# Optimization experiments

Hardware: AMD Instinct MI355X
Metric: run time of the kernel (lower is better)

The kernel has to match this reference:

```python
import jax, jax.numpy as jnp
import numpy as np

WINDOW = (2, 7, 7)
SHIFT = (1, 3, 3)
HEADS = 4


def _rel_pos_index(ws):
    coords = np.stack(np.meshgrid(*[np.arange(w) for w in ws], indexing='ij'))  # (3, wd, wh, ww)
    cf = coords.reshape(3, -1)
    rel = cf[:, :, None] - cf[:, None, :]  # (3, N, N)
    rel = rel.transpose(1, 2, 0).astype(np.int64)
    rel[:, :, 0] += ws[0] - 1
    rel[:, :, 1] += ws[1] - 1
    rel[:, :, 2] += ws[2] - 1
    rel[:, :, 0] *= (2 * ws[1] - 1) * (2 * ws[2] - 1)
    rel[:, :, 1] *= 2 * ws[2] - 1
    return rel.sum(-1)  # (N, N)


def _attn_mask(D, H, W, ws, ss):
    img = np.zeros((1, D, H, W, 1), np.float32)
    cnt = 0
    for d in (slice(None, -ws[0]), slice(-ws[0], -ss[0]), slice(-ss[0], None)):
        for h in (slice(None, -ws[1]), slice(-ws[1], -ss[1]), slice(-ss[1], None)):
            for w in (slice(None, -ws[2]), slice(-ws[2], -ss[2]), slice(-ss[2], None)):
                img[:, d, h, w, :] = cnt
                cnt += 1
    N = ws[0] * ws[1] * ws[2]
    mw = img.reshape(1, D // ws[0], ws[0], H // ws[1], ws[1], W // ws[2], ws[2], 1)
    mw = mw.transpose(0, 1, 3, 5, 2, 4, 6, 7).reshape(-1, N)  # (nW, N)
    diff = mw[:, None, :] - mw[:, :, None]
    return np.where(diff != 0, -100.0, 0.0).astype(np.float32)  # (nW, N, N)


def _win_partition(x, ws):
    B, D, H, W, C = x.shape
    x = x.reshape(B, D // ws[0], ws[0], H // ws[1], ws[1], W // ws[2], ws[2], C)
    return x.transpose(0, 1, 3, 5, 2, 4, 6, 7).reshape(-1, ws[0] * ws[1] * ws[2], C)


def _win_reverse(win, ws, B, D, H, W):
    C = win.shape[-1]
    x = win.reshape(B, D // ws[0], H // ws[1], W // ws[2], ws[0], ws[1], ws[2], C)
    return x.transpose(0, 1, 4, 2, 5, 3, 6, 7).reshape(B, D, H, W, C)


def _ln(x, w, b):
    mu = x.mean(-1, keepdims=True)
    var = x.var(-1, keepdims=True)
    return (x - mu) / jnp.sqrt(var + 1e-5) * w + b


def setup_inputs() -> dict:
    key = jax.random.key(0)
    ks = jax.random.split(key, 8)
    B, D, H, W, C = 4, 8, 56, 56, 128
    hidden = 4 * C
    table = (2 * WINDOW[0] - 1) * (2 * WINDOW[1] - 1) * (2 * WINDOW[2] - 1)
    return {
        'x': jax.random.normal(ks[0], (B, D, H, W, C), jnp.float32),
        'norm1_w': jnp.ones((C,), jnp.float32),
        'norm1_b': jnp.zeros((C,), jnp.float32),
        'qkv_w': 0.02 * jax.random.normal(ks[1], (3 * C, C), jnp.float32),
        'qkv_b': jnp.zeros((3 * C,), jnp.float32),
        'rpb': 0.02 * jax.random.normal(ks[2], (table, HEADS), jnp.float32),
        'proj_w': 0.02 * jax.random.normal(ks[3], (C, C), jnp.float32),
        'proj_b': jnp.zeros((C,), jnp.float32),
        'norm2_w': jnp.ones((C,), jnp.float32),
        'norm2_b': jnp.zeros((C,), jnp.float32),
        'fc1_w': 0.02 * jax.random.normal(ks[4], (hidden, C), jnp.float32),
        'fc1_b': jnp.zeros((hidden,), jnp.float32),
        'fc2_w': 0.02 * jax.random.normal(ks[5], (C, hidden), jnp.float32),
        'fc2_b': jnp.zeros((C,), jnp.float32),
    }


def reference(x, norm1_w, norm1_b, qkv_w, qkv_b, rpb, proj_w, proj_b,
              norm2_w, norm2_b, fc1_w, fc1_b, fc2_w, fc2_b):
    B, D, H, W, C = x.shape
    hd = C // HEADS
    scale = hd ** -0.5
    N = WINDOW[0] * WINDOW[1] * WINDOW[2]

    shortcut = x
    y = _ln(x, norm1_w, norm1_b)
    # cyclic shift (SW-MSA)
    y = jnp.roll(y, (-SHIFT[0], -SHIFT[1], -SHIFT[2]), axis=(1, 2, 3))
    win = _win_partition(y, WINDOW)  # (B_, N, C)
    B_ = win.shape[0]

    qkv = win @ qkv_w.T + qkv_b  # (B_, N, 3C)
    qkv = qkv.reshape(B_, N, 3, HEADS, hd).transpose(2, 0, 3, 1, 4)
    q, k, v = qkv[0] * scale, qkv[1], qkv[2]  # (B_, h, N, hd)

    attn = jnp.einsum('bhnd,bhmd->bhnm', q, k)  # (B_, h, N, N)
    rpi = _rel_pos_index(WINDOW)
    bias = rpb[rpi.reshape(-1)].reshape(N, N, HEADS).transpose(2, 0, 1)  # (h, N, N)
    attn = attn + bias[None]

    mask = jnp.asarray(_attn_mask(D, H, W, WINDOW, SHIFT))  # (nW, N, N)
    nW = mask.shape[0]
    attn = attn.reshape(B_ // nW, nW, HEADS, N, N) + mask[None, :, None]
    attn = jax.nn.softmax(attn.reshape(B_, HEADS, N, N), axis=-1)

    out = jnp.einsum('bhnm,bhmd->bhnd', attn, v)
    out = out.transpose(0, 2, 1, 3).reshape(B_, N, C)
    out = out @ proj_w.T + proj_b

    y = _win_reverse(out, WINDOW, B, D, H, W)
    y = jnp.roll(y, SHIFT, axis=(1, 2, 3))  # reverse cyclic shift
    x = shortcut + y

    h = _ln(x, norm2_w, norm2_b)
    h = jax.nn.gelu(h @ fc1_w.T + fc1_b, approximate=False)
    h = h @ fc2_w.T + fc2_b
    return x + h
```

## Files before the change

### kernel.cpp

```cpp
#include <hip/hip_runtime.h>
#include <math.h>

typedef short bf16x8 __attribute__((ext_vector_type(8)));
typedef float f32x4 __attribute__((ext_vector_type(4)));
typedef unsigned short u16;

#define DEVFN static __device__ __forceinline__

DEVFN u16 f2bf(float f) {
  union { float f; unsigned u; } v; v.f = f;
  return (u16)((v.u + 0x7FFFu + ((v.u >> 16) & 1u)) >> 16);
}

DEVFN void gload16(const void* g, void* l) {
  __builtin_amdgcn_global_load_lds(
      (const __attribute__((address_space(1))) void*)g,
      (__attribute__((address_space(3))) void*)l, 16, 0, 0);
}

DEVFN float gelu_fast(float x) {
  float e = __expf(-1.702f * x);
  return x * __builtin_amdgcn_rcpf(1.0f + e);
}

#define TT 100352
#define BWIN 1024

__global__ void convert4_kernel(const float* __restrict__ a, const float* __restrict__ b,
                                const float* __restrict__ c, const float* __restrict__ d,
                                u16* __restrict__ oa, u16* __restrict__ ob,
                                u16* __restrict__ oc, u16* __restrict__ od) {
  int i = blockIdx.x * 256 + threadIdx.x;
  const float* s; u16* o; int off;
  if (i < 49152)       { s = a; o = oa; off = i; }
  else if (i < 65536)  { s = b; o = ob; off = i - 49152; }
  else if (i < 131072) { s = c; o = oc; off = i - 65536; }
  else                 { s = d; o = od; off = i - 131072; }
  o[off] = f2bf(s[off]);
}

__global__ void biasmask_kernel(const float* __restrict__ rpb, float* __restrict__ bm) {
  int idx = blockIdx.x * 256 + threadIdx.x;
  int lane = idx & 63;
  int rem = idx >> 6;
  int nt = rem % 7;  rem /= 7;
  int mt = rem % 7;  rem /= 7;
  int h = rem & 3;
  int pat = rem >> 2;
  int dB = (pat >> 2) & 1, hB = (pat >> 1) & 1, wB = pat & 1;
  int jc = nt * 16 + (lane & 15);
  f32x4 out;
  #pragma unroll
  for (int r = 0; r < 4; ++r) {
    int ic = mt * 16 + (lane >> 4) * 4 + r;
    float v;
    if (jc > 97) v = -30000.f;
    else if (ic > 97) v = 0.f;
    else {
      int di = ic / 49, ri = ic % 49, hi = ri / 7, wi = ri % 7;
      int dj = jc / 49, rj = jc % 49, hj = rj / 7, wj = rj % 7;
      int tidx = (di - dj + 1) * 169 + (hi - hj + 6) * 13 + (wi - wj + 6);
      v = rpb[tidx * 4 + h];
      int ridi = (dB ? (di == 0 ? 1 : 2) * 9 : 0) + (hB ? (hi < 4 ? 1 : 2) * 3 : 0)
               + (wB ? (wi < 4 ? 1 : 2) : 0);
      int ridj = (dB ? (dj == 0 ? 1 : 2) * 9 : 0) + (hB ? (hj < 4 ? 1 : 2) * 3 : 0)
               + (wB ? (wj < 4 ? 1 : 2) : 0);
      if (ridi != ridj) v -= 100.f;
    }
    out[r] = v;
  }
  *(f32x4*)(bm + (size_t)idx * 4) = out;
}

__global__ __launch_bounds__(256) void ln_kernel(const float* __restrict__ x,
    const float* __restrict__ w, const float* __restrict__ bterm, u16* __restrict__ out)
{
  int gw = blockIdx.x * 4 + (threadIdx.x >> 6);
  int lane = threadIdx.x & 63;
  int b_ = gw / 98, n = gw % 98;
  int bb = b_ >> 8, widx = b_ & 255;
  int dw = widx >> 6, hw = (widx >> 3) & 7, ww = widx & 7;
  int dd = n / 49, rr = n % 49, hh = rr / 7, wn = rr % 7;
  int d = (dw * 2 + dd + 1) & 7;
  int h = hw * 7 + hh + 3; if (h >= 56) h -= 56;
  int wq = ww * 7 + wn + 3; if (wq >= 56) wq -= 56;
  size_t src = ((size_t)(((bb * 8 + d) * 56 + h) * 56 + wq)) * 128;
  float2 v = *(const float2*)(x + src + lane * 2);
  float s = v.x + v.y, q = v.x * v.x + v.y * v.y;
  #pragma unroll
  for (int m = 1; m < 64; m <<= 1) { s += __shfl_xor(s, m, 64); q += __shfl_xor(q, m, 64); }
  float mu = s * (1.0f / 128.0f);
  float var = q * (1.0f / 128.0f) - mu * mu;
  float rstd = rsqrtf(var + 1e-5f);
  int c = lane * 2;
  float y0 = (v.x - mu) * rstd * w[c] + bterm[c];
  float y1 = (v.y - mu) * rstd * w[c + 1] + bterm[c + 1];
  ushort2 o; o.x = f2bf(y0); o.y = f2bf(y1);
  *(ushort2*)(out + (size_t)gw * 128 + c) = o;
}

template<int EPI>
__global__ __launch_bounds__(256) void gemm_kernel(
    const u16* __restrict__ A, const u16* __restrict__ Bw,
    const float* __restrict__ bias, const float* __restrict__ res,
    void* __restrict__ outp, const float* __restrict__ n2w,
    const float* __restrict__ n2b, u16* __restrict__ h1out,
    int M, int N, int K)
{
  __shared__ u16 smem[EPI == 1 ? 17664 : 16384];
  u16* As = smem;
  u16* Bs = smem + 8192;
  const int m0 = blockIdx.x * 128, n0 = blockIdx.y * 128;
  const int t = threadIdx.x;
  const int wid = t >> 6, lane = t & 63;
  const int wr = wid >> 1, wc = wid & 1;
  const int l15 = lane & 15, lhi = lane >> 4;
  const int srow = lane >> 3;
  const int sslot = lane & 7;
  const int gcol = ((sslot ^ srow) << 3);
  f32x4 acc[4][4] = {};
  for (int k0 = 0; k0 < K; k0 += 64) {
    #pragma unroll
    for (int it = 0; it < 4; ++it) {
      const int rbase = it * 32 + wid * 8;
      const int row = rbase + srow;
      gload16(A + (size_t)(m0 + row) * K + k0 + gcol, As + rbase * 64);
      gload16(Bw + (size_t)(n0 + row) * K + k0 + gcol, Bs + rbase * 64);
    }
    __syncthreads();
    #pragma unroll
    for (int kk = 0; kk < 64; kk += 32) {
      bf16x8 af[4], bfr[4];
      const int csw = (kk + lhi * 8) ^ ((l15 & 7) << 3);
      #pragma unroll
      for (int mi = 0; mi < 4; ++mi) af[mi] = *(const bf16x8*)(As + (wr * 64 + mi * 16 + l15) * 64 + csw);
      #pragma unroll
      for (int ni = 0; ni < 4; ++ni) bfr[ni] = *(const bf16x8*)(Bs + (wc * 64 + ni * 16 + l15) * 64 + csw);
      #pragma unroll
      for (int mi = 0; mi < 4; ++mi)
        #pragma unroll
        for (int ni = 0; ni < 4; ++ni)
          acc[mi][ni] = __builtin_amdgcn_mfma_f32_16x16x32_bf16(af[mi], bfr[ni], acc[mi][ni], 0, 0, 0);
    }
    __syncthreads();
  }
  if (EPI == 0) {
    const float smul = (n0 == 0) ? 0.17677669529663689f : 1.0f;
    #pragma unroll
    for (int mi = 0; mi < 4; ++mi)
      #pragma unroll
      for (int ni = 0; ni < 4; ++ni) {
        int col = wc * 64 + ni * 16 + l15;
        float bcol = bias[n0 + col];
        #pragma unroll
        for (int r = 0; r < 4; ++r) {
          int row = wr * 64 + mi * 16 + lhi * 4 + r;
          float v = (acc[mi][ni][r] + bcol) * smul;
          smem[row * 128 + (((col >> 3) ^ (row & 7)) << 3) + (col & 7)] = f2bf(v);
        }
      }
    __syncthreads();
    const int rsub = t >> 4, sl = t & 15;
    #pragma unroll
    for (int j = 0; j < 8; ++j) {
      int row = j * 16 + rsub;
      int4 val = *(const int4*)(smem + row * 128 + ((sl ^ (row & 7)) << 3));
      *(int4*)((u16*)outp + (size_t)(m0 + row) * N + n0 + sl * 8) = val;
    }
  } else {
    float* Pk = (float*)smem;
    #pragma unroll
    for (int half = 0; half < 2; ++half) {
      if (wr == half) {
        #pragma unroll
        for (int ni = 0; ni < 4; ++ni) {
          int col = wc * 64 + ni * 16 + l15;
          float bcol = bias[col];
          #pragma unroll
          for (int mi = 0; mi < 4; ++mi)
            #pragma unroll
            for (int r = 0; r < 4; ++r)
              Pk[(mi * 16 + lhi * 4 + r) * 138 + col] = acc[mi][ni][r] + bcol;
        }
      }
      __syncthreads();
      {
        int rowl = t >> 2, q = t & 3;
        int grow = m0 + half * 64 + rowl;
        int b_ = grow / 98, n = grow % 98;
        int bb = b_ >> 8, widx = b_ & 255;
        int dw = widx >> 6, hw = (widx >> 3) & 7, ww = widx & 7;
        int dd = n / 49, rr = n % 49, hh = rr / 7, wn = rr % 7;
        int d = (dw * 2 + dd + 1) & 7;
        int hq = hw * 7 + hh + 3; if (hq >= 56) hq -= 56;
        int wq = ww * 7 + wn + 3; if (wq >= 56) wq -= 56;
        size_t dbase = ((size_t)(((bb * 8 + d) * 56 + hq) * 56 + wq)) * 128;
        f32x4 vals[8];
        float s = 0.f, sq = 0.f;
        #pragma unroll
        for (int j = 0; j < 8; ++j) {
          int col = j * 16 + q * 4;
          f32x4 pv = *(const f32x4*)(Pk + rowl * 138 + col);
          f32x4 rv = *(const f32x4*)(res + dbase + col);
          f32x4 v = pv + rv;
          vals[j] = v;
          *(f32x4*)((float*)outp + dbase + col) = v;
          s += v[0] + v[1] + v[2] + v[3];
          sq += v[0]*v[0] + v[1]*v[1] + v[2]*v[2] + v[3]*v[3];
        }
        s += __shfl_xor(s, 1, 64);  sq += __shfl_xor(sq, 1, 64);
        s += __shfl_xor(s, 2, 64);  sq += __shfl_xor(sq, 2, 64);
        float mu = s * (1.0f / 128.0f);
        float var = sq * (1.0f / 128.0f) - mu * mu;
        float rstd = rsqrtf(var + 1e-5f);
        #pragma unroll
        for (int j = 0; j < 8; ++j) {
          int col = j * 16 + q * 4;
          f32x4 wv = *(const f32x4*)(n2w + col);
          f32x4 bv = *(const f32x4*)(n2b + col);
          u16 hb[4];
          #pragma unroll
          for (int e = 0; e < 4; ++e)
            hb[e] = f2bf((vals[j][e] - mu) * rstd * wv[e] + bv[e]);
          *(int2*)(h1out + dbase + col) = *(const int2*)hb;
        }
      }
      __syncthreads();
    }
  }
}

__global__ __launch_bounds__(256, 2) void mlp_kernel(
    const u16* __restrict__ A, const u16* __restrict__ W1, const float* __restrict__ b1,
    const u16* __restrict__ W2, const float* __restrict__ b2,
    const float* __restrict__ res, float* __restrict__ outp)
{
  __shared__ u16 smem[34816];
  u16* W1c = smem;
  u16* W2c = smem + 8192;
  u16* HsA = smem + 24576;
  float* b1s = (float*)(smem + 33792);
  float* Pk = (float*)smem;
  const int m0 = blockIdx.x * 128;
  const int t = threadIdx.x, wid = t >> 6, lane = t & 63;
  const int l15 = lane & 15, lhi = lane >> 4;
  const int srow4 = lane >> 4, sslot16 = lane & 15;
  const int srow8 = lane >> 3, sslot8 = lane & 7;
  u16* hs = HsA + wid * 2304;

  #pragma unroll
  for (int it = 0; it < 4; ++it) {
    int rb1 = it * 16 + wid * 4, r1 = rb1 + srow4;
    gload16(W1 + (size_t)r1 * 128 + ((sslot16 ^ (r1 & 7)) << 3), W1c + rb1 * 128);
    int rb2 = it * 32 + wid * 8, r2 = rb2 + srow8;
    gload16(W2 + (size_t)r2 * 512 + ((sslot8 ^ (r2 & 7)) << 3), W2c + rb2 * 64);
  }
  if (t < 128) *(f32x4*)(b1s + t * 4) = *(const f32x4*)(b1 + t * 4);
  bf16x8 areg[2][4];
  #pragma unroll
  for (int mi = 0; mi < 2; ++mi)
    #pragma unroll
    for (int kg = 0; kg < 4; ++kg)
      areg[mi][kg] = *(const bf16x8*)(A + (size_t)(m0 + wid * 32 + mi * 16 + l15) * 128 + kg * 32 + lhi * 8);

  f32x4 accO[2][8] = {};
  __syncthreads();
  for (int hc = 0; hc < 8; ++hc) {
    const int cur = (hc & 1) * 8192;
    if (hc < 7) {
      const int nxt = ((hc + 1) & 1) * 8192;
      #pragma unroll
      for (int it = 0; it < 4; ++it) {
        int rb2 = it * 32 + wid * 8, r2 = rb2 + srow8;
        gload16(W2 + (size_t)r2 * 512 + (hc + 1) * 64 + ((sslot8 ^ (r2 & 7)) << 3),
                W2c + nxt + rb2 * 64);
      }
    }
    f32x4 accH[2][4] = {};
    #pragma unroll
    for (int kk = 0; kk < 4; ++kk) {
      bf16x8 bw[4];
      #pragma unroll
      for (int ni = 0; ni < 4; ++ni) {
        int row = ni * 16 + l15;
        bw[ni] = *(const bf16x8*)(W1c + row * 128 + (((kk * 4 + lhi) ^ (row & 7)) << 3));
      }
      #pragma unroll
      for (int mi = 0; mi < 2; ++mi)
        #pragma unroll
        for (int ni = 0; ni < 4; ++ni)
          accH[mi][ni] = __builtin_amdgcn_mfma_f32_16x16x32_bf16(areg[mi][kk], bw[ni], accH[mi][ni], 0, 0, 0);
    }
    #pragma unroll
    for (int mi = 0; mi < 2; ++mi)
      #pragma unroll
      for (int ni = 0; ni < 4; ++ni) {
        float bb = b1s[hc * 64 + ni * 16 + l15];
        #pragma unroll
        for (int r = 0; r < 4; ++r) {
          int tokl = mi * 16 + lhi * 4 + r;
          hs[tokl * 72 + ni * 16 + l15] = f2bf(gelu_fast(accH[mi][ni][r] + bb));
        }
      }
    __syncthreads();
    if (hc < 7) {
      #pragma unroll
      for (int it = 0; it < 4; ++it) {
        int rb1 = it * 16 + wid * 4, r1 = rb1 + srow4;
        gload16(W1 + (size_t)((hc + 1) * 64 + r1) * 128 + ((sslot16 ^ (r1 & 7)) << 3),
                W1c + rb1 * 128);
      }
    }
    #pragma unroll
    for (int kk = 0; kk < 2; ++kk) {
      bf16x8 ah[2], bw2[8];
      #pragma unroll
      for (int mi = 0; mi < 2; ++mi)
        ah[mi] = *(const bf16x8*)(hs + (mi * 16 + l15) * 72 + kk * 32 + lhi * 8);
      #pragma unroll
      for (int ni = 0; ni < 8; ++ni) {
        int row = ni * 16 + l15;
        bw2[ni] = *(const bf16x8*)(W2c + cur + row * 64 + (((kk * 4 + lhi) ^ (row & 7)) << 3));
      }
      #pragma unroll
      for (int mi = 0; mi < 2; ++mi)
        #pragma unroll
        for (int ni = 0; ni < 8; ++ni)
          accO[mi][ni] = __builtin_amdgcn_mfma_f32_16x16x32_bf16(ah[mi], bw2[ni], accO[mi][ni], 0, 0, 0);
    }
    __syncthreads();
  }
  #pragma unroll
  for (int half = 0; half < 2; ++half) {
    if ((wid >> 1) == half) {
      #pragma unroll
      for (int ni = 0; ni < 8; ++ni) {
        int col = ni * 16 + l15;
        float bv = b2[col];
        #pragma unroll
        for (int mi = 0; mi < 2; ++mi)
          #pragma unroll
          for (int r = 0; r < 4; ++r) {
            int tokl = (wid & 1) * 32 + mi * 16 + lhi * 4 + r;
            Pk[tokl * 132 + col] = accO[mi][ni][r] + bv;
          }
      }
    }
    __syncthreads();
    #pragma unroll
    for (int p = 0; p < 8; ++p) {
      int idx = p * 256 + t;
      int row = idx >> 5, c = (idx & 31) * 4;
      size_t gtok = (size_t)(m0 + half * 64 + row);
      f32x4 v = *(const f32x4*)(Pk + row * 132 + c);
      f32x4 rv = *(const f32x4*)(res + gtok * 128 + c);
      *(f32x4*)(outp + gtok * 128 + c) = v + rv;
    }
    __syncthreads();
  }
}

__global__ __launch_bounds__(64) void attn_kernel(
    const u16* __restrict__ qkv, const float* __restrict__ biasmask,
    u16* __restrict__ out_win)
{
  __shared__ u16 vT[32][136];
  __shared__ u16 P[16][136];
  const int bid = blockIdx.x;
  const int w = bid >> 2, h = bid & 3;
  const int lane = threadIdx.x;
  const int l15 = lane & 15, lhi = lane >> 4;
  const int widx = w & 255;
  const int dw = widx >> 6, hw = (widx >> 3) & 7, ww = widx & 7;
  const int pat = ((dw == 3) ? 4 : 0) | ((hw == 7) ? 2 : 0) | ((ww == 7) ? 1 : 0);
  const float* bmh = biasmask + (size_t)(pat * 4 + h) * (49 * 256);

  for (int f = lane; f < 160; f += 64) {
    int d = f / 5, c = 96 + (f % 5) * 8;
    *(int4*)&vT[d][c] = (int4){0, 0, 0, 0};
  }
  if (lane < 48) {
    int r = lane / 3, c = 112 + (lane % 3) * 8;
    *(int4*)&P[r][c] = (int4){0, 0, 0, 0};
  }
  const size_t base = (size_t)w * 98 * 384;
  for (int f = lane; f < 392; f += 64) {
    int n = f >> 2, c = (f & 3) * 8;
    int4 v = *(const int4*)(qkv + base + (size_t)n * 384 + 256 + h * 32 + c);
    const u16* pv = (const u16*)&v;
    #pragma unroll
    for (int j = 0; j < 8; ++j) vT[c + j][n] = pv[j];
  }
  const size_t obase = (size_t)w * 98 * 128;
  for (int mt = 0; mt < 7; ++mt) {
    int qn = mt * 16 + l15; if (qn > 97) qn = 97;
    bf16x8 aq = *(const bf16x8*)(qkv + base + (size_t)qn * 384 + h * 32 + lhi * 8);
    f32x4 sf[7];
    #pragma unroll
    for (int nt = 0; nt < 7; ++nt) {
      int kn = nt * 16 + l15; if (kn > 97) kn = 97;
      bf16x8 bk = *(const bf16x8*)(qkv + base + (size_t)kn * 384 + 128 + h * 32 + lhi * 8);
      f32x4 z = {0.f, 0.f, 0.f, 0.f};
      sf[nt] = __builtin_amdgcn_mfma_f32_16x16x32_bf16(aq, bk, z, 0, 0, 0);
    }
    float mx[4] = {-1e30f, -1e30f, -1e30f, -1e30f};
    #pragma unroll
    for (int nt = 0; nt < 7; ++nt) {
      f32x4 bm = *(const f32x4*)(bmh + (mt * 7 + nt) * 256 + lane * 4);
      #pragma unroll
      for (int r = 0; r < 4; ++r) {
        float s = sf[nt][r] + bm[r];
        sf[nt][r] = s;
        mx[r] = fmaxf(mx[r], s);
      }
    }
    #pragma unroll
    for (int m = 1; m < 16; m <<= 1)
      #pragma unroll
      for (int r = 0; r < 4; ++r) mx[r] = fmaxf(mx[r], __shfl_xor(mx[r], m, 64));
    float sm[4] = {0.f, 0.f, 0.f, 0.f};
    #pragma unroll
    for (int nt = 0; nt < 7; ++nt)
      #pragma unroll
      for (int r = 0; r < 4; ++r) {
        float p = __expf(sf[nt][r] - mx[r]);
        sf[nt][r] = p;
        sm[r] += p;
      }
    #pragma unroll
    for (int m = 1; m < 16; m <<= 1)
      #pragma unroll
      for (int r = 0; r < 4; ++r) sm[r] += __shfl_xor(sm[r], m, 64);
    float inv[4];
    #pragma unroll
    for (int r = 0; r < 4; ++r) inv[r] = 1.0f / sm[r];
    #pragma unroll
    for (int nt = 0; nt < 7; ++nt)
      #pragma unroll
      for (int r = 0; r < 4; ++r)
        P[lhi * 4 + r][nt * 16 + l15] = f2bf(sf[nt][r] * inv[r]);
    f32x4 o0 = {}, o1 = {};
    #pragma unroll
    for (int ks = 0; ks < 4; ++ks) {
      bf16x8 ap  = *(const bf16x8*)(&P[l15][ks * 32 + lhi * 8]);
      bf16x8 bv0 = *(const bf16x8*)(&vT[l15][ks * 32 + lhi * 8]);
      bf16x8 bv1 = *(const bf16x8*)(&vT[16 + l15][ks * 32 + lhi * 8]);
      o0 = __builtin_amdgcn_mfma_f32_16x16x32_bf16(ap, bv0, o0, 0, 0, 0);
      o1 = __builtin_amdgcn_mfma_f32_16x16x32_bf16(ap, bv1, o1, 0, 0, 0);
    }
    int irow0 = mt * 16 + lhi * 4;
    #pragma unroll
    for (int r = 0; r < 4; ++r) {
      if (irow0 + r < 98) {
        size_t orow = obase + (size_t)(irow0 + r) * 128 + h * 32;
        out_win[orow + l15] = f2bf(o0[r]);
        out_win[orow + 16 + l15] = f2bf(o1[r]);
      }
    }
  }
}

extern "C" void kernel_launch(void* const* d_in, const int* in_sizes, int n_in,
                              void* d_out, int out_size, void* d_ws, size_t ws_size,
                              hipStream_t stream)
{
  const float* x      = (const float*)d_in[0];
  const float* n1w    = (const float*)d_in[1];
  const float* n1b    = (const float*)d_in[2];
  const float* qkv_w  = (const float*)d_in[3];
  const float* qkv_b  = (const float*)d_in[4];
  const float* rpb    = (const float*)d_in[5];
  const float* proj_w = (const float*)d_in[6];
  const float* proj_b = (const float*)d_in[7];
  const float* n2w    = (const float*)d_in[8];
  const float* n2b    = (const float*)d_in[9];
  const float* fc1_w  = (const float*)d_in[10];
  const float* fc1_b  = (const float*)d_in[11];
  const float* fc2_w  = (const float*)d_in[12];
  const float* fc2_b  = (const float*)d_in[13];

  char* p = (char*)d_ws;
  size_t off = 0;
  auto alloc = [&](size_t bytes) { void* r = p + off; off = (off + bytes + 255) & ~(size_t)255; return r; };
  u16*   qkvw_b    = (u16*)alloc(49152 * 2);
  u16*   projw_b   = (u16*)alloc(16384 * 2);
  u16*   fc1w_b    = (u16*)alloc(65536 * 2);
  u16*   fc2w_b    = (u16*)alloc(65536 * 2);
  float* biasmask  = (float*)alloc(8 * 4 * 49 * 256 * 4);
  u16*   y_win     = (u16*)alloc((size_t)TT * 128 * 2);
  float* x2        = (float*)alloc((size_t)TT * 128 * 4);
  u16*   h1        = (u16*)alloc((size_t)TT * 128 * 2);
  u16*   big       = (u16*)alloc((size_t)TT * 384 * 2);
  if (off > ws_size) return;

  convert4_kernel<<<768, 256, 0, stream>>>(qkv_w, proj_w, fc1_w, fc2_w,
                                           qkvw_b, projw_b, fc1w_b, fc2w_b);
  biasmask_kernel<<<392, 256, 0, stream>>>(rpb, biasmask);
  ln_kernel<<<TT / 4, 256, 0, stream>>>(x, n1w, n1b, y_win);
  gemm_kernel<0><<<dim3(TT / 128, 3), 256, 0, stream>>>(y_win, qkvw_b, qkv_b, nullptr, big,
                                                        nullptr, nullptr, nullptr, TT, 384, 128);
  attn_kernel<<<BWIN * 4, 64, 0, stream>>>(big, biasmask, y_win);
  gemm_kernel<1><<<dim3(TT / 128, 1), 256, 0, stream>>>(y_win, projw_b, proj_b, x, x2,
                                                        n2w, n2b, h1, TT, 128, 128);
  mlp_kernel<<<TT / 128, 256, 0, stream>>>(h1, fc1w_b, fc1_b, fc2w_b, fc2_b, x2, (float*)d_out);
}
```

Before: 199.7 us.

## Fuse LayerNorm1 into QKV GEMM and store residual x2 in bf16

Removes the standalone LayerNorm kernel: the QKV GEMM now gathers the shifted-window rows of x, normalizes them in registers and writes the bf16 A tile directly into shared memory. Each of the three column blocks recomputes the same LayerNorm, trading extra fp32 reads of x for skipping a separate pass and the y_win round trip. Separately, the intermediate residual x2 is stored as bf16 instead of fp32, halving its write and read traffic at a precision cost in the final residual add.

```diff
diff --git a/kernel.cpp b/kernel.cpp
--- a/kernel.cpp
+++ b/kernel.cpp
@@ -10,6 +10,11 @@
 DEVFN u16 f2bf(float f) {
   union { float f; unsigned u; } v; v.f = f;
   return (u16)((v.u + 0x7FFFu + ((v.u >> 16) & 1u)) >> 16);
+}
+
+DEVFN float bf2f(u16 u) {
+  union { unsigned u; float f; } v; v.u = ((unsigned)u) << 16;
+  return v.f;
 }
 
 DEVFN void gload16(const void* g, void* l) {
@@ -72,44 +77,13 @@
   *(f32x4*)(bm + (size_t)idx * 4) = out;
 }
 
-__global__ __launch_bounds__(256) void ln_kernel(const float* __restrict__ x,
-    const float* __restrict__ w, const float* __restrict__ bterm, u16* __restrict__ out)
+__global__ __launch_bounds__(256) void qkv_kernel(
+    const float* __restrict__ x, const float* __restrict__ n1w, const float* __restrict__ n1b,
+    const u16* __restrict__ Bw, const float* __restrict__ bias, u16* __restrict__ outp)
 {
-  int gw = blockIdx.x * 4 + (threadIdx.x >> 6);
-  int lane = threadIdx.x & 63;
-  int b_ = gw / 98, n = gw % 98;
-  int bb = b_ >> 8, widx = b_ & 255;
-  int dw = widx >> 6, hw = (widx >> 3) & 7, ww = widx & 7;
-  int dd = n / 49, rr = n % 49, hh = rr / 7, wn = rr % 7;
-  int d = (dw * 2 + dd + 1) & 7;
-  int h = hw * 7 + hh + 3; if (h >= 56) h -= 56;
-  int wq = ww * 7 + wn + 3; if (wq >= 56) wq -= 56;
-  size_t src = ((size_t)(((bb * 8 + d) * 56 + h) * 56 + wq)) * 128;
-  float2 v = *(const float2*)(x + src + lane * 2);
-  float s = v.x + v.y, q = v.x * v.x + v.y * v.y;
-  #pragma unroll
-  for (int m = 1; m < 64; m <<= 1) { s += __shfl_xor(s, m, 64); q += __shfl_xor(q, m, 64); }
-  float mu = s * (1.0f / 128.0f);
-  float var = q * (1.0f / 128.0f) - mu * mu;
-  float rstd = rsqrtf(var + 1e-5f);
-  int c = lane * 2;
-  float y0 = (v.x - mu) * rstd * w[c] + bterm[c];
-  float y1 = (v.y - mu) * rstd * w[c + 1] + bterm[c + 1];
-  ushort2 o; o.x = f2bf(y0); o.y = f2bf(y1);
-  *(ushort2*)(out + (size_t)gw * 128 + c) = o;
-}
-
-template<int EPI>
-__global__ __launch_bounds__(256) void gemm_kernel(
-    const u16* __restrict__ A, const u16* __restrict__ Bw,
-    const float* __restrict__ bias, const float* __restrict__ res,
-    void* __restrict__ outp, const float* __restrict__ n2w,
-    const float* __restrict__ n2b, u16* __restrict__ h1out,
-    int M, int N, int K)
-{
-  __shared__ u16 smem[EPI == 1 ? 17664 : 16384];
+  __shared__ u16 smem[24576];
   u16* As = smem;
-  u16* Bs = smem + 8192;
+  u16* Bs = smem + 16384;
   const int m0 = blockIdx.x * 128, n0 = blockIdx.y * 128;
   const int t = threadIdx.x;
   const int wid = t >> 6, lane = t & 63;
@@ -118,14 +92,127 @@
   const int srow = lane >> 3;
   const int sslot = lane & 7;
   const int gcol = ((sslot ^ srow) << 3);
+
+  {
+    const int rowl = t >> 1, half = t & 1;
+    const int grow = m0 + rowl;
+    int b_ = grow / 98, n = grow % 98;
+    int bb = b_ >> 8, widx = b_ & 255;
+    int dwv = widx >> 6, hwv = (widx >> 3) & 7, wwv = widx & 7;
+    int dd = n / 49, rr = n % 49, hh = rr / 7, wn = rr % 7;
+    int d = (dwv * 2 + dd + 1) & 7;
+    int hq = hwv * 7 + hh + 3; if (hq >= 56) hq -= 56;
+    int wq = wwv * 7 + wn + 3; if (wq >= 56) wq -= 56;
+    size_t src = ((size_t)(((bb * 8 + d) * 56 + hq) * 56 + wq)) * 128 + half * 64;
+    f32x4 vals[16];
+    float s = 0.f, sq = 0.f;
+    #pragma unroll
+    for (int j = 0; j < 16; ++j) {
+      f32x4 v = *(const f32x4*)(x + src + j * 4);
+      vals[j] = v;
+      s += v[0] + v[1] + v[2] + v[3];
+      sq += v[0]*v[0] + v[1]*v[1] + v[2]*v[2] + v[3]*v[3];
+    }
+    s += __shfl_xor(s, 1, 64);  sq += __shfl_xor(sq, 1, 64);
+    float mu = s * (1.0f / 128.0f);
+    float var = sq * (1.0f / 128.0f) - mu * mu;
+    float rstd = rsqrtf(var + 1e-5f);
+    #pragma unroll
+    for (int j = 0; j < 8; ++j) {
+      int col = half * 64 + j * 8;
+      f32x4 wv0 = *(const f32x4*)(n1w + col);
+      f32x4 wv1 = *(const f32x4*)(n1w + col + 4);
+      f32x4 bv0 = *(const f32x4*)(n1b + col);
+      f32x4 bv1 = *(const f32x4*)(n1b + col + 4);
+      u16 hb[8];
+      #pragma unroll
+      for (int e = 0; e < 4; ++e) {
+        hb[e]     = f2bf((vals[2*j][e]   - mu) * rstd * wv0[e] + bv0[e]);
+        hb[e + 4] = f2bf((vals[2*j+1][e] - mu) * rstd * wv1[e] + bv1[e]);
+      }
+      *(bf16x8*)(As + rowl * 128 + ((((col >> 3) ^ (rowl & 7))) << 3)) = *(const bf16x8*)hb;
+    }
+  }
+
   f32x4 acc[4][4] = {};
-  for (int k0 = 0; k0 < K; k0 += 64) {
+  for (int k0 = 0; k0 < 128; k0 += 64) {
     #pragma unroll
     for (int it = 0; it < 4; ++it) {
       const int rbase = it * 32 + wid * 8;
       const int row = rbase + srow;
-      gload16(A + (size_t)(m0 + row) * K + k0 + gcol, As + rbase * 64);
-      gload16(Bw + (size_t)(n0 + row) * K + k0 + gcol, Bs + rbase * 64);
+      gload16(Bw + (size_t)(n0 + row) * 128 + k0 + gcol, Bs + rbase * 64);
+    }
+    __syncthreads();
+    #pragma unroll
+    for (int kk = 0; kk < 64; kk += 32) {
+      bf16x8 af[4], bfr[4];
+      const int cg = ((k0 + kk) >> 3) + lhi;
+      const int csw = (kk + lhi * 8) ^ ((l15 & 7) << 3);
+      #pragma unroll
+      for (int mi = 0; mi < 4; ++mi) {
+        int row = wr * 64 + mi * 16 + l15;
+        af[mi] = *(const bf16x8*)(As + row * 128 + ((cg ^ (row & 7)) << 3));
+      }
+      #pragma unroll
+      for (int ni = 0; ni < 4; ++ni)
+        bfr[ni] = *(const bf16x8*)(Bs + (wc * 64 + ni * 16 + l15) * 64 + csw);
+      #pragma unroll
+      for (int mi = 0; mi < 4; ++mi)
+        #pragma unroll
+        for (int ni = 0; ni < 4; ++ni)
+          acc[mi][ni] = __builtin_amdgcn_mfma_f32_16x16x32_bf16(af[mi], bfr[ni], acc[mi][ni], 0, 0, 0);
+    }
+    __syncthreads();
+  }
+  const float smul = (n0 == 0) ? 0.17677669529663689f : 1.0f;
+  #pragma unroll
+  for (int mi = 0; mi < 4; ++mi)
+    #pragma unroll
+    for (int ni = 0; ni < 4; ++ni) {
+      int col = wc * 64 + ni * 16 + l15;
+      float bcol = bias[n0 + col];
+      #pragma unroll
+      for (int r = 0; r < 4; ++r) {
+        int row = wr * 64 + mi * 16 + lhi * 4 + r;
+        float v = (acc[mi][ni][r] + bcol) * smul;
+        smem[row * 128 + (((col >> 3) ^ (row & 7)) << 3) + (col & 7)] = f2bf(v);
+      }
+    }
+  __syncthreads();
+  const int rsub = t >> 4, sl = t & 15;
+  #pragma unroll
+  for (int j = 0; j < 8; ++j) {
+    int row = j * 16 + rsub;
+    int4 val = *(const int4*)(smem + row * 128 + ((sl ^ (row & 7)) << 3));
+    *(int4*)(outp + (size_t)(m0 + row) * 384 + n0 + sl * 8) = val;
+  }
+}
+
+__global__ __launch_bounds__(256) void proj_kernel(
+    const u16* __restrict__ A, const u16* __restrict__ Bw,
+    const float* __restrict__ bias, const float* __restrict__ res,
+    u16* __restrict__ x2out, const float* __restrict__ n2w,
+    const float* __restrict__ n2b, u16* __restrict__ h1out)
+{
+  __shared__ u16 smem[17664];
+  u16* As = smem;
+  u16* Bs = smem + 8192;
+  const int m0 = blockIdx.x * 128;
+  const int t = threadIdx.x;
+  const int wid = t >> 6, lane = t & 63;
+  const int wr = wid >> 1, wc = wid & 1;
+  const int l15 = lane & 15, lhi = lane >> 4;
+  const int srow = lane >> 3;
+  const int sslot = lane & 7;
+  const int gcol = ((sslot ^ srow) << 3);
+  f32x4 acc[4][4] = {};
+  for (int k0 = 0; k0 < 128; k0 += 64) {
+    #pragma unroll
+    for (int it = 0; it < 4; ++it) {
+      const int rbase = it * 32 + wid * 8;
+      const int row = rbase + srow;
+      gload16(A + (size_t)(m0 + row) * 128 + k0 + gcol, As + rbase * 64);
+      gload16(Bw + (size_t)row * 128 + k0 + gcol, Bs + rbase * 64);
     }
     __syncthreads();
     #pragma unroll
@@ -144,96 +231,73 @@
     }
     __syncthreads();
   }
-  if (EPI == 0) {
-    const float smul = (n0 == 0) ? 0.17677669529663689f : 1.0f;
-    #pragma unroll
-    for (int mi = 0; mi < 4; ++mi)
+  float* Pk = (float*)smem;
+  #pragma unroll
+  for (int half = 0; half < 2; ++half) {
+    if (wr == half) {
       #pragma unroll
       for (int ni = 0; ni < 4; ++ni) {
         int col = wc * 64 + ni * 16 + l15;
-        float bcol = bias[n0 + col];
-        #pragma unroll
-        for (int r = 0; r < 4; ++r) {
-          int row = wr * 64 + mi * 16 + lhi * 4 + r;
-          float v = (acc[mi][ni][r] + bcol) * smul;
-          smem[row * 128 + (((col >> 3) ^ (row & 7)) << 3) + (col & 7)] = f2bf(v);
+        float bcol = bias[col];
+        #pragma unroll
+        for (int mi = 0; mi < 4; ++mi)
+          #pragma unroll
+          for (int r = 0; r < 4; ++r)
+            Pk[(mi * 16 + lhi * 4 + r) * 138 + col] = acc[mi][ni][r] + bcol;
+      }
+    }
+    __syncthreads();
+    {
+      int rowl = t >> 2, q = t & 3;
+      int grow = m0 + half * 64 + rowl;
+      int b_ = grow / 98, n = grow % 98;
+      int bb = b_ >> 8, widx = b_ & 255;
+      int dw = widx >> 6, hw = (widx >> 3) & 7, ww = widx & 7;
+      int dd = n / 49, rr = n % 49, hh = rr / 7, wn = rr % 7;
+      int d = (dw * 2 + dd + 1) & 7;
+      int hq = hw * 7 + hh + 3; if (hq >= 56) hq -= 56;
+      int wq = ww * 7 + wn + 3; if (wq >= 56) wq -= 56;
+      size_t dbase = ((size_t)(((bb * 8 + d) * 56 + hq) * 56 + wq)) * 128;
+      f32x4 vals[8];
+      float s = 0.f, sq = 0.f;
+      #pragma unroll
+      for (int j = 0; j < 8; ++j) {
+        int col = j * 16 + q * 4;
+        f32x4 pv = *(const f32x4*)(Pk + rowl * 138 + col);
+        f32x4 rv = *(const f32x4*)(res + dbase + col);
+        f32x4 v = pv + rv;
+        vals[j] = v;
+        s += v[0] + v[1] + v[2] + v[3];
+        sq += v[0]*v[0] + v[1]*v[1] + v[2]*v[2] + v[3]*v[3];
+      }
+      s += __shfl_xor(s, 1, 64);  sq += __shfl_xor(sq, 1, 64);
+      s += __shfl_xor(s, 2, 64);  sq += __shfl_xor(sq, 2, 64);
+      float mu = s * (1.0f / 128.0f);
+      float var = sq * (1.0f / 128.0f) - mu * mu;
+      float rstd = rsqrtf(var + 1e-5f);
+      #pragma unroll
+      for (int j = 0; j < 8; ++j) {
+        int col = j * 16 + q * 4;
+        f32x4 wv = *(const f32x4*)(n2w + col);
+        f32x4 bv = *(const f32x4*)(n2b + col);
+        u16 xb[4], hb[4];
+        #pragma unroll
+        for (int e = 0; e < 4; ++e) {
+          xb[e] = f2bf(vals[j][e]);
+          hb[e] = f2bf((vals[j][e] - mu) * rstd * wv[e] + bv[e]);
         }
-      }
-    __syncthreads();
-    const int rsub = t >> 4, sl = t & 15;
-    #pragma unroll
-    for (int j = 0; j < 8; ++j) {
-      int row = j * 16 + rsub;
-      int4 val = *(const int4*)(smem + row * 128 + ((sl ^ (row & 7)) << 3));
-      *(int4*)((u16*)outp + (size_t)(m0 + row) * N + n0 + sl * 8) = val;
-    }
-  } else {
-    float* Pk = (float*)smem;
-    #pragma unroll
-    for (int half = 0; half < 2; ++half) {
-      if (wr == half) {
-        #pragma unroll
-        for (int ni = 0; ni < 4; ++ni) {
-          int col = wc * 64 + ni * 16 + l15;
-          float bcol = bias[col];
-          #pragma unroll
-          for (int mi = 0; mi < 4; ++mi)
-            #pragma unroll
-            for (int r = 0; r < 4; ++r)
-              Pk[(mi * 16 + lhi * 4 + r) * 138 + col] = acc[mi][ni][r] + bcol;
-        }
-      }
-      __syncthreads();
-      {
-        int rowl = t >> 2, q = t & 3;
-        int grow = m0 + half * 64 + rowl;
-        int b_ = grow / 98, n = grow % 98;
-        int bb = b_ >> 8, widx = b_ & 255;
-        int dw = widx >> 6, hw = (widx >> 3) & 7, ww = widx & 7;
-        int dd = n / 49, rr = n % 49, hh = rr / 7, wn = rr % 7;
-        int d = (dw * 2 + dd + 1) & 7;
-        int hq = hw * 7 + hh + 3; if (hq >= 56) hq -= 56;
-        int wq = ww * 7 + wn + 3; if (wq >= 56) wq -= 56;
-        size_t dbase = ((size_t)(((bb * 8 + d) * 56 + hq) * 56 + wq)) * 128;
-        f32x4 vals[8];
-        float s = 0.f, sq = 0.f;
-        #pragma unroll
-        for (int j = 0; j < 8; ++j) {
-          int col = j * 16 + q * 4;
-          f32x4 pv = *(const f32x4*)(Pk + rowl * 138 + col);
-          f32x4 rv = *(const f32x4*)(res + dbase + col);
-          f32x4 v = pv + rv;
-          vals[j] = v;
-          *(f32x4*)((float*)outp + dbase + col) = v;
-          s += v[0] + v[1] + v[2] + v[3];
-          sq += v[0]*v[0] + v[1]*v[1] + v[2]*v[2] + v[3]*v[3];
-        }
-        s += __shfl_xor(s, 1, 64);  sq += __shfl_xor(sq, 1, 64);
-        s += __shfl_xor(s, 2, 64);  sq += __shfl_xor(sq, 2, 64);
-        float mu = s * (1.0f / 128.0f);
-        float var = sq * (1.0f / 128.0f) - mu * mu;
-        float rstd = rsqrtf(var + 1e-5f);
-        #pragma unroll
-        for (int j = 0; j < 8; ++j) {
-          int col = j * 16 + q * 4;
-          f32x4 wv = *(const f32x4*)(n2w + col);
-          f32x4 bv = *(const f32x4*)(n2b + col);
-          u16 hb[4];
-          #pragma unroll
-          for (int e = 0; e < 4; ++e)
-            hb[e] = f2bf((vals[j][e] - mu) * rstd * wv[e] + bv[e]);
-          *(int2*)(h1out + dbase + col) = *(const int2*)hb;
-        }
-      }
-      __syncthreads();
-    }
+        *(int2*)(x2out + dbase + col) = *(const int2*)xb;
+        *(int2*)(h1out + dbase + col) = *(const int2*)hb;
+      }
+    }
+    __syncthreads();
   }
 }
 
 __global__ __launch_bounds__(256, 2) void mlp_kernel(
     const u16* __restrict__ A, const u16* __restrict__ W1, const float* __restrict__ b1,
     const u16* __restrict__ W2, const float* __restrict__ b2,
-    const float* __restrict__ res, float* __restrict__ outp)
+    const u16* __restrict__ res, float* __restrict__ outp)
 {
   __shared__ u16 smem[34816];
   u16* W1c = smem;
@@ -353,7 +417,10 @@
       int row = idx >> 5, c = (idx & 31) * 4;
       size_t gtok = (size_t)(m0 + half * 64 + row);
       f32x4 v = *(const f32x4*)(Pk + row * 132 + c);
-      f32x4 rv = *(const f32x4*)(res + gtok * 128 + c);
+      short4 rb = *(const short4*)(res + gtok * 128 + c);
+      f32x4 rv;
+      rv[0] = bf2f((u16)rb.x); rv[1] = bf2f((u16)rb.y);
+      rv[2] = bf2f((u16)rb.z); rv[3] = bf2f((u16)rb.w);
       *(f32x4*)(outp + gtok * 128 + c) = v + rv;
     }
     __syncthreads();
@@ -488,7 +555,7 @@
   u16*   fc2w_b    = (u16*)alloc(65536 * 2);
   float* biasmask  = (float*)alloc(8 * 4 * 49 * 256 * 4);
   u16*   y_win     = (u16*)alloc((size_t)TT * 128 * 2);
-  float* x2        = (float*)alloc((size_t)TT * 128 * 4);
+  u16*   x2        = (u16*)alloc((size_t)TT * 128 * 2);
   u16*   h1        = (u16*)alloc((size_t)TT * 128 * 2);
   u16*   big       = (u16*)alloc((size_t)TT * 384 * 2);
   if (off > ws_size) return;
@@ -496,11 +563,8 @@
   convert4_kernel<<<768, 256, 0, stream>>>(qkv_w, proj_w, fc1_w, fc2_w,
                                            qkvw_b, projw_b, fc1w_b, fc2w_b);
   biasmask_kernel<<<392, 256, 0, stream>>>(rpb, biasmask);
-  ln_kernel<<<TT / 4, 256, 0, stream>>>(x, n1w, n1b, y_win);
-  gemm_kernel<0><<<dim3(TT / 128, 3), 256, 0, stream>>>(y_win, qkvw_b, qkv_b, nullptr, big,
-                                                        nullptr, nullptr, nullptr, TT, 384, 128);
+  qkv_kernel<<<dim3(TT / 128, 3), 256, 0, stream>>>(x, n1w, n1b, qkvw_b, qkv_b, big);
   attn_kernel<<<BWIN * 4, 64, 0, stream>>>(big, biasmask, y_win);
-  gemm_kernel<1><<<dim3(TT / 128, 1), 256, 0, stream>>>(y_win, projw_b, proj_b, x, x2,
-                                                        n2w, n2b, h1, TT, 128, 128);
+  proj_kernel<<<TT / 128, 256, 0, stream>>>(y_win, projw_b, proj_b, x, x2, n2w, n2b, h1);
   mlp_kernel<<<TT / 128, 256, 0, stream>>>(h1, fc1w_b, fc1_b, fc2w_b, fc2_b, x2, (float*)d_out);
 }
```

Result: slower. 206.5 us (+3.4%).
